# Performance work log

Hardware: AMD Instinct MI355X
Metric: run time of the kernel (lower is better)

The kernel has to match this reference:

```python
import jax, jax.numpy as jnp
import numpy as np

N_NODES = 200000
N_EDGES = 3200000
IN_DIM = 16
EMB_DIM = 8


def setup_inputs() -> dict:
    key = jax.random.key(0)
    ks = jax.random.split(key, 8)
    x = jax.random.normal(ks[0], (N_NODES, IN_DIM), dtype=jnp.float32)
    edge_index = jax.random.randint(ks[1], (2, N_EDGES), 0, N_NODES, dtype=jnp.int32)
    edge_weight = jax.random.uniform(ks[2], (N_EDGES,), dtype=jnp.float32)
    W1_l = jax.random.normal(ks[3], (EMB_DIM, IN_DIM), dtype=jnp.float32) / np.sqrt(IN_DIM)
    W1_r = jax.random.normal(ks[4], (EMB_DIM, IN_DIM), dtype=jnp.float32) / np.sqrt(IN_DIM)
    b1 = jnp.zeros((EMB_DIM,), dtype=jnp.float32)
    W3_l = jax.random.normal(ks[5], (EMB_DIM, EMB_DIM), dtype=jnp.float32) / np.sqrt(EMB_DIM)
    W3_r = jax.random.normal(ks[6], (EMB_DIM, EMB_DIM), dtype=jnp.float32) / np.sqrt(EMB_DIM)
    b3 = jnp.zeros((EMB_DIM,), dtype=jnp.float32)
    return {"x": x, "edge_index": edge_index, "edge_weight": edge_weight,
            "W1_l": W1_l, "W1_r": W1_r, "b1": b1,
            "W3_l": W3_l, "W3_r": W3_r, "b3": b3}


def _sage_conv(x, src, dst, w, W_l, W_r, b):
    # weighted message: x_j * edge_weight, mean-aggregated over in-degree
    n = x.shape[0]
    msg = x[src] * w[:, None]                                  # [E, F]
    agg = jax.ops.segment_sum(msg, dst, num_segments=n)        # [N, F]
    cnt = jax.ops.segment_sum(jnp.ones_like(w), dst, num_segments=n)
    mean = agg / jnp.maximum(cnt, 1.0)[:, None]
    return mean @ W_l.T + x @ W_r.T + b


def reference(x, edge_index, edge_weight, W1_l, W1_r, b1, W3_l, W3_r, b3):
    src, dst = edge_index[0], edge_index[1]
    h = _sage_conv(x, src, dst, edge_weight, W1_l, W1_r, b1)
    h = jax.nn.relu(h)
    # dropout is identity in eval mode
    h = _sage_conv(h, src, dst, edge_weight, W3_l, W3_r, b3)
    return jax.nn.log_softmax(h, axis=1)
```

## Files before the change

kernel.cpp:

```cpp
#include <hip/hip_runtime.h>
#include <hip/hip_fp16.h>
#include <math.h>

#define NN 200000
#define NE 3200000
#define IN_DIM 16
#define EMB 8
#define BK 256
#define NBUK ((NN + BK - 1) / BK)
#define NBLK ((NN + 255) / 256)
#define PLACE_BLOCKS 512
#define PLACE_T 512
#define CHUNK (NE / PLACE_BLOCKS)
#define EPT 13
#define AGG_T 1024
#define CAP 5120
#define RPT 5
#define PRE 4

typedef float vf4 __attribute__((ext_vector_type(4)));
typedef int   vi2 __attribute__((ext_vector_type(2)));

__device__ __forceinline__ void gacc(float* acc, const __half* p, unsigned r)
{
    float w = (float)(r & 63u) * 0.015625f;
    int s = (int)((r >> 6) & 0x3FFFFu);
    vf4 g = *(const vf4*)(p + (size_t)s * EMB);
    union { vf4 f; __half2 h[4]; } u; u.f = g;
    float2 a = __half22float2(u.h[0]);
    float2 c = __half22float2(u.h[1]);
    float2 d = __half22float2(u.h[2]);
    float2 e = __half22float2(u.h[3]);
    acc[0] = fmaf(a.x, w, acc[0]);
    acc[1] = fmaf(a.y, w, acc[1]);
    acc[2] = fmaf(c.x, w, acc[2]);
    acc[3] = fmaf(c.y, w, acc[3]);
    acc[4] = fmaf(d.x, w, acc[4]);
    acc[5] = fmaf(d.y, w, acc[5]);
    acc[6] = fmaf(e.x, w, acc[6]);
    acc[7] = fmaf(e.y, w, acc[7]);
}

__global__ __launch_bounds__(256) void k_init(
    const float* __restrict__ x,
    const float* __restrict__ W1l,
    const float* __restrict__ W1r,
    const float* __restrict__ b1,
    __half* __restrict__ pA, float* __restrict__ t,
    int* __restrict__ bcur)
{
    __shared__ float sWl[EMB * IN_DIM];
    __shared__ float sWr[EMB * IN_DIM];
    __shared__ float sb[EMB];
    int tid = threadIdx.x;
    if (tid < EMB * IN_DIM) { sWl[tid] = W1l[tid]; sWr[tid] = W1r[tid]; }
    if (tid < EMB) sb[tid] = b1[tid];
    __syncthreads();

    int i = blockIdx.x * blockDim.x + tid;
    if (i < NBUK) bcur[i] = i * CAP;
    if (i >= NN) return;

    float xi[IN_DIM];
    const float4* xp = (const float4*)(x + (size_t)i * IN_DIM);
    #pragma unroll
    for (int q = 0; q < 4; ++q) {
        float4 v = xp[q];
        xi[4*q+0] = v.x; xi[4*q+1] = v.y; xi[4*q+2] = v.z; xi[4*q+3] = v.w;
    }

    float pe[EMB], te[EMB];
    #pragma unroll
    for (int e = 0; e < EMB; ++e) {
        float sp = 0.f, st = sb[e];
        #pragma unroll
        for (int k = 0; k < IN_DIM; ++k) {
            sp = fmaf(xi[k], sWl[e * IN_DIM + k], sp);
            st = fmaf(xi[k], sWr[e * IN_DIM + k], st);
        }
        pe[e] = sp; te[e] = st;
    }

    union { vf4 f; __half2 h[4]; } up;
    up.h[0] = __floats2half2_rn(pe[0], pe[1]);
    up.h[1] = __floats2half2_rn(pe[2], pe[3]);
    up.h[2] = __floats2half2_rn(pe[4], pe[5]);
    up.h[3] = __floats2half2_rn(pe[6], pe[7]);
    *(vf4*)(pA + (size_t)i * EMB) = up.f;

    vf4* tp = (vf4*)(t + (size_t)i * EMB);
    vf4 t0 = {te[0], te[1], te[2], te[3]};
    vf4 t1 = {te[4], te[5], te[6], te[7]};
    tp[0] = t0;
    tp[1] = t1;
}

__global__ __launch_bounds__(PLACE_T) void k_bplace(
    const int* __restrict__ src, const int* __restrict__ dst,
    const float* __restrict__ w,
    int* __restrict__ bcur, unsigned* __restrict__ recs)
{
    __shared__ int h[NBUK];
    __shared__ int lb[NBUK];
    __shared__ int gb[NBUK];
    __shared__ int sv[8];
    __shared__ unsigned srec[CHUNK];
    __shared__ unsigned short sbkt[CHUNK];

    int tid = threadIdx.x;
    for (int i = tid; i < NBUK; i += PLACE_T) h[i] = 0;
    __syncthreads();

    int e0 = blockIdx.x * CHUNK;
    int e1 = e0 + CHUNK;

    unsigned rec[EPT];
    int rb[EPT];
    #pragma unroll
    for (int k = 0; k < EPT; ++k) {
        int e = e0 + tid + k * PLACE_T;
        rb[k] = -1;
        if (e < e1) {
            int d = dst[e];
            int b = d >> 8;
            int rank = atomicAdd(&h[b], 1);
            unsigned kq = __float2uint_rn(w[e] * 64.f);
            if (kq > 63u) kq = 63u;
            rec[k] = ((unsigned)(d & (BK - 1)) << 24) | ((unsigned)src[e] << 6) | kq;
            rb[k] = (b << 16) | rank;
        }
    }
    __syncthreads();

    {
        int base2 = tid * 2;
        int s0 = 0, s1 = 0, tot = 0;
        if (base2 + 0 < NBUK) { s0 = tot; tot += h[base2 + 0]; }
        if (base2 + 1 < NBUK) { s1 = tot; tot += h[base2 + 1]; }
        int lane = tid & 63;
        int incl = tot;
        #pragma unroll
        for (int o = 1; o < 64; o <<= 1) {
            int v = __shfl_up(incl, o);
            if (lane >= o) incl += v;
        }
        if (lane == 63) sv[tid >> 6] = incl;
        __syncthreads();
        int wid = tid >> 6;
        int wbase = 0;
        #pragma unroll
        for (int ww = 0; ww < 7; ++ww)
            if (ww < wid) wbase += sv[ww];
        int excl = wbase + incl - tot;
        if (base2 + 0 < NBUK) lb[base2 + 0] = excl + s0;
        if (base2 + 1 < NBUK) lb[base2 + 1] = excl + s1;
    }
    __syncthreads();

    for (int i = tid; i < NBUK; i += PLACE_T) {
        int c = h[i];
        gb[i] = c ? atomicAdd(bcur + i, c) : 0;
    }

    #pragma unroll
    for (int k = 0; k < EPT; ++k) {
        if (rb[k] >= 0) {
            int b = rb[k] >> 16;
            int pos = lb[b] + (rb[k] & 0xFFFF);
            srec[pos] = rec[k];
            sbkt[pos] = (unsigned short)b;
        }
    }
    __syncthreads();

    for (int j = tid; j < CHUNK; j += PLACE_T) {
        int b = sbkt[j];
        recs[gb[b] + (j - lb[b])] = srec[j];
    }
}

__global__ __launch_bounds__(AGG_T) void k_agg1(
    unsigned* __restrict__ recs, const int* __restrict__ bcur,
    const __half* __restrict__ pA, float* __restrict__ t,
    const float* __restrict__ W3l, const float* __restrict__ W3r,
    const float* __restrict__ b3,
    __half* __restrict__ pB, float* __restrict__ invdeg,
    int* __restrict__ soff, int* __restrict__ sdeg)
{
    __shared__ unsigned sbuf[CAP];
    __shared__ int shist[BK];
    __shared__ int sval[4];
    __shared__ int soffl[BK + 1];
    __shared__ float sWl[EMB * EMB];
    __shared__ float sWr[EMB * EMB];
    __shared__ float sb[EMB];

    int tid = threadIdx.x;
    int b = blockIdx.x;
    int bb = b * CAP;
    int cnt = bcur[b] - bb;

    if (tid < EMB * EMB) { sWl[tid] = W3l[tid]; sWr[tid] = W3r[tid]; }
    if (tid < EMB) sb[tid] = b3[tid];
    if (tid < BK) shist[tid] = 0;
    __syncthreads();

    unsigned rec[RPT];
    int rdl[RPT];
    #pragma unroll
    for (int k = 0; k < RPT; ++k) {
        int j = tid + k * AGG_T;
        rdl[k] = -1;
        if (j < cnt) {
            unsigned r = recs[bb + j];
            int dl = (int)(r >> 24);
            int rank = atomicAdd(&shist[dl], 1);
            rec[k] = r;
            rdl[k] = (dl << 16) | rank;
        }
    }
    __syncthreads();

    {
        int v = (tid < BK) ? shist[tid] : 0;
        int lane = tid & 63;
        int incl = v;
        #pragma unroll
        for (int o = 1; o < 64; o <<= 1) {
            int vv = __shfl_up(incl, o);
            if (lane >= o) incl += vv;
        }
        if (tid < BK && lane == 63) sval[tid >> 6] = incl;
        __syncthreads();
        if (tid < BK) {
            int wid = tid >> 6;
            int wbase = 0;
            #pragma unroll
            for (int ww = 0; ww < 3; ++ww)
                if (ww < wid) wbase += sval[ww];
            soffl[tid] = wbase + incl - v;
        }
        if (tid == 0) soffl[BK] = cnt;
    }
    __syncthreads();

    #pragma unroll
    for (int k = 0; k < RPT; ++k) {
        if (rdl[k] >= 0) {
            int dl = rdl[k] >> 16;
            sbuf[soffl[dl] + (rdl[k] & 0xFFFF)] = rec[k];
        }
    }
    __syncthreads();

    for (int p = tid; 2 * p < cnt; p += AGG_T) {
        vi2 q;
        q.x = (int)sbuf[2 * p];
        q.y = (2 * p + 1 < cnt) ? (int)sbuf[2 * p + 1] : 0;
        *(vi2*)(recs + bb + 2 * p) = q;
    }

    int dl = tid >> 2;
    int quarter = tid & 3;
    int i = b * BK + dl;
    bool valid = (i < NN);
    float acc[EMB] = {0.f, 0.f, 0.f, 0.f, 0.f, 0.f, 0.f, 0.f};
    int r0 = 0, r1 = 0;
    if (valid) {
        r0 = soffl[dl];
        r1 = soffl[dl + 1];
        unsigned rr[PRE];
        #pragma unroll
        for (int k = 0; k < PRE; ++k) {
            int j = r0 + quarter + 4 * k;
            rr[k] = (j < r1) ? sbuf[j] : 0u;
        }
        #pragma unroll
        for (int k = 0; k < PRE; ++k) {
            int j = r0 + quarter + 4 * k;
            if (j < r1) gacc(acc, pA, rr[k]);
        }
        for (int j = r0 + quarter + 4 * PRE; j < r1; j += 4) {
            gacc(acc, pA, sbuf[j]);
        }
    }
    #pragma unroll
    for (int e = 0; e < EMB; ++e) {
        acc[e] += __shfl_xor(acc[e], 1);
        acc[e] += __shfl_xor(acc[e], 2);
    }
    if (!valid || quarter) return;

    int deg = r1 - r0;
    soff[i] = bb + r0;
    sdeg[i] = deg;
    float inv = 1.0f / fmaxf((float)deg, 1.0f);
    invdeg[i] = inv;

    vf4* tp = (vf4*)(t + (size_t)i * EMB);
    vf4 t0 = tp[0], t1 = tp[1];

    float h[EMB];
    h[0] = fmaxf(fmaf(acc[0], inv, t0.x), 0.f);
    h[1] = fmaxf(fmaf(acc[1], inv, t0.y), 0.f);
    h[2] = fmaxf(fmaf(acc[2], inv, t0.z), 0.f);
    h[3] = fmaxf(fmaf(acc[3], inv, t0.w), 0.f);
    h[4] = fmaxf(fmaf(acc[4], inv, t1.x), 0.f);
    h[5] = fmaxf(fmaf(acc[5], inv, t1.y), 0.f);
    h[6] = fmaxf(fmaf(acc[6], inv, t1.z), 0.f);
    h[7] = fmaxf(fmaf(acc[7], inv, t1.w), 0.f);

    float pe[EMB], te[EMB];
    #pragma unroll
    for (int o = 0; o < EMB; ++o) {
        float sp = 0.f, st = sb[o];
        #pragma unroll
        for (int k = 0; k < EMB; ++k) {
            sp = fmaf(h[k], sWl[o * EMB + k], sp);
            st = fmaf(h[k], sWr[o * EMB + k], st);
        }
        pe[o] = sp; te[o] = st;
    }

    union { vf4 f; __half2 h2[4]; } up;
    up.h2[0] = __floats2half2_rn(pe[0], pe[1]);
    up.h2[1] = __floats2half2_rn(pe[2], pe[3]);
    up.h2[2] = __floats2half2_rn(pe[4], pe[5]);
    up.h2[3] = __floats2half2_rn(pe[6], pe[7]);
    *(vf4*)(pB + (size_t)i * EMB) = up.f;

    vf4 s0 = {te[0], te[1], te[2], te[3]};
    vf4 s1 = {te[4], te[5], te[6], te[7]};
    tp[0] = s0;
    tp[1] = s1;
}

__global__ __launch_bounds__(256) void k_agg2(
    const unsigned* __restrict__ recs, const int* __restrict__ soff,
    const int* __restrict__ sdeg,
    const __half* __restrict__ pB, const float* __restrict__ t,
    const float* __restrict__ invdeg,
    float* __restrict__ out)
{
    int gid = blockIdx.x * 256 + threadIdx.x;
    int i = gid >> 2;
    int quarter = gid & 3;
    if (i >= NN) return;

    int r0 = soff[i];
    int r1 = r0 + sdeg[i];
    float acc[EMB] = {0.f, 0.f, 0.f, 0.f, 0.f, 0.f, 0.f, 0.f};

    unsigned rr[PRE];
    #pragma unroll
    for (int k = 0; k < PRE; ++k) {
        int j = r0 + quarter + 4 * k;
        rr[k] = (j < r1) ? recs[j] : 0u;
    }
    #pragma unroll
    for (int k = 0; k < PRE; ++k) {
        int j = r0 + quarter + 4 * k;
        if (j < r1) gacc(acc, pB, rr[k]);
    }
    for (int j = r0 + quarter + 4 * PRE; j < r1; j += 4) {
        gacc(acc, pB, recs[j]);
    }

    #pragma unroll
    for (int e = 0; e < EMB; ++e) {
        acc[e] += __shfl_xor(acc[e], 1);
        acc[e] += __shfl_xor(acc[e], 2);
    }
    if (quarter) return;

    float inv = invdeg[i];
    const vf4* tp = (const vf4*)(t + (size_t)i * EMB);
    vf4 t0 = tp[0], t1 = tp[1];

    float z[EMB];
    z[0] = fmaf(acc[0], inv, t0.x);
    z[1] = fmaf(acc[1], inv, t0.y);
    z[2] = fmaf(acc[2], inv, t0.z);
    z[3] = fmaf(acc[3], inv, t0.w);
    z[4] = fmaf(acc[4], inv, t1.x);
    z[5] = fmaf(acc[5], inv, t1.y);
    z[6] = fmaf(acc[6], inv, t1.z);
    z[7] = fmaf(acc[7], inv, t1.w);

    float m = z[0];
    #pragma unroll
    for (int k = 1; k < EMB; ++k) m = fmaxf(m, z[k]);
    float s = 0.f;
    #pragma unroll
    for (int k = 0; k < EMB; ++k) s += expf(z[k] - m);
    float ls = m + logf(s);

    vf4* op = (vf4*)(out + (size_t)i * EMB);
    vf4 o0 = {z[0]-ls, z[1]-ls, z[2]-ls, z[3]-ls};
    vf4 o1 = {z[4]-ls, z[5]-ls, z[6]-ls, z[7]-ls};
    op[0] = o0;
    op[1] = o1;
}

extern "C" void kernel_launch(void* const* d_in, const int* in_sizes, int n_in,
                              void* d_out, int out_size, void* d_ws, size_t ws_size,
                              hipStream_t stream)
{
    const float* x   = (const float*)d_in[0];
    const int*   ei  = (const int*)d_in[1];
    const float* ew  = (const float*)d_in[2];
    const float* W1l = (const float*)d_in[3];
    const float* W1r = (const float*)d_in[4];
    const float* b1  = (const float*)d_in[5];
    const float* W3l = (const float*)d_in[6];
    const float* W3r = (const float*)d_in[7];
    const float* b3  = (const float*)d_in[8];
    float* out = (float*)d_out;

    const int* src = ei;
    const int* dst = ei + NE;

    char* w = (char*)d_ws;
    float*    t     = (float*)w;     w += (size_t)NN * EMB * 4;
    __half*   pA    = (__half*)w;    w += (size_t)NN * EMB * 2;
    __half*   pB    = (__half*)w;    w += (size_t)NN * EMB * 2;
    float*    invd  = (float*)w;     w += (size_t)NN * 4;
    int*      soff  = (int*)w;       w += (size_t)NN * 4;
    int*      sdeg  = (int*)w;       w += (size_t)NN * 4;
    int*      bcur  = (int*)w;       w += (size_t)NBUK * 4;
    w = (char*)(((size_t)w + 15) & ~(size_t)15);
    unsigned* recs  = (unsigned*)w;

    dim3 blk(256);

    k_init<<<dim3(NBLK), blk, 0, stream>>>(x, W1l, W1r, b1, pA, t, bcur);
    k_bplace<<<dim3(PLACE_BLOCKS), dim3(PLACE_T), 0, stream>>>(src, dst, ew, bcur, recs);
    k_agg1<<<dim3(NBUK), dim3(AGG_T), 0, stream>>>(recs, bcur, pA, t, W3l, W3r, b3, pB, invd, soff, sdeg);
    k_agg2<<<dim3((4 * NN + 255) / 256), blk, 0, stream>>>(recs, soff, sdeg, pB, t, invd, out);
}
```

Before: 96.66 us.

## Fuse layer-1 node projection into edge placement and widen agg2 to 8 lanes

The per-node layer-1 projections (pA, t) move out of the separate init kernel and into the bucket-placement kernel, so each placement block also processes its own slice of nodes and only a tiny one-block kernel remains to initialise bucket cursors. This aims to overlap the dense node work with the edge scatter and remove a full-grid launch. Separately, the second aggregation now gives each node 8 lanes instead of 4, with a shallower prefetch and an extra shuffle stage, to raise memory-level parallelism on the gathers. The cost is more threads and more reduction work for low-degree nodes, plus extra registers and shared memory in the placement kernel.

Result: slower. 126.5 us (+30.9%).

```diff
diff --git a/kernel.cpp b/kernel.cpp
--- a/kernel.cpp
+++ b/kernel.cpp
@@ -8,15 +8,16 @@
 #define EMB 8
 #define BK 256
 #define NBUK ((NN + BK - 1) / BK)
-#define NBLK ((NN + 255) / 256)
 #define PLACE_BLOCKS 512
 #define PLACE_T 512
 #define CHUNK (NE / PLACE_BLOCKS)
 #define EPT 13
+#define NPB ((NN + PLACE_BLOCKS - 1) / PLACE_BLOCKS)
 #define AGG_T 1024
 #define CAP 5120
 #define RPT 5
 #define PRE 4
+#define PRE2 2
 
 typedef float vf4 __attribute__((ext_vector_type(4)));
 typedef int   vi2 __attribute__((ext_vector_type(2)));
@@ -41,74 +42,35 @@
     acc[7] = fmaf(e.y, w, acc[7]);
 }
 
-__global__ __launch_bounds__(256) void k_init(
-    const float* __restrict__ x,
-    const float* __restrict__ W1l,
-    const float* __restrict__ W1r,
-    const float* __restrict__ b1,
-    __half* __restrict__ pA, float* __restrict__ t,
-    int* __restrict__ bcur)
-{
-    __shared__ float sWl[EMB * IN_DIM];
-    __shared__ float sWr[EMB * IN_DIM];
-    __shared__ float sb[EMB];
-    int tid = threadIdx.x;
-    if (tid < EMB * IN_DIM) { sWl[tid] = W1l[tid]; sWr[tid] = W1r[tid]; }
-    if (tid < EMB) sb[tid] = b1[tid];
-    __syncthreads();
-
-    int i = blockIdx.x * blockDim.x + tid;
+__global__ __launch_bounds__(1024) void k_zero(int* __restrict__ bcur)
+{
+    int i = threadIdx.x;
     if (i < NBUK) bcur[i] = i * CAP;
-    if (i >= NN) return;
-
-    float xi[IN_DIM];
-    const float4* xp = (const float4*)(x + (size_t)i * IN_DIM);
-    #pragma unroll
-    for (int q = 0; q < 4; ++q) {
-        float4 v = xp[q];
-        xi[4*q+0] = v.x; xi[4*q+1] = v.y; xi[4*q+2] = v.z; xi[4*q+3] = v.w;
-    }
-
-    float pe[EMB], te[EMB];
-    #pragma unroll
-    for (int e = 0; e < EMB; ++e) {
-        float sp = 0.f, st = sb[e];
-        #pragma unroll
-        for (int k = 0; k < IN_DIM; ++k) {
-            sp = fmaf(xi[k], sWl[e * IN_DIM + k], sp);
-            st = fmaf(xi[k], sWr[e * IN_DIM + k], st);
-        }
-        pe[e] = sp; te[e] = st;
-    }
-
-    union { vf4 f; __half2 h[4]; } up;
-    up.h[0] = __floats2half2_rn(pe[0], pe[1]);
-    up.h[1] = __floats2half2_rn(pe[2], pe[3]);
-    up.h[2] = __floats2half2_rn(pe[4], pe[5]);
-    up.h[3] = __floats2half2_rn(pe[6], pe[7]);
-    *(vf4*)(pA + (size_t)i * EMB) = up.f;
-
-    vf4* tp = (vf4*)(t + (size_t)i * EMB);
-    vf4 t0 = {te[0], te[1], te[2], te[3]};
-    vf4 t1 = {te[4], te[5], te[6], te[7]};
-    tp[0] = t0;
-    tp[1] = t1;
 }
 
 __global__ __launch_bounds__(PLACE_T) void k_bplace(
     const int* __restrict__ src, const int* __restrict__ dst,
     const float* __restrict__ w,
+    const float* __restrict__ x,
+    const float* __restrict__ W1l, const float* __restrict__ W1r,
+    const float* __restrict__ b1,
+    __half* __restrict__ pA, float* __restrict__ t,
     int* __restrict__ bcur, unsigned* __restrict__ recs)
 {
     __shared__ int h[NBUK];
     __shared__ int lb[NBUK];
     __shared__ int gb[NBUK];
     __shared__ int sv[8];
+    __shared__ float sWl[EMB * IN_DIM];
+    __shared__ float sWr[EMB * IN_DIM];
+    __shared__ float sb[EMB];
     __shared__ unsigned srec[CHUNK];
     __shared__ unsigned short sbkt[CHUNK];
 
     int tid = threadIdx.x;
     for (int i = tid; i < NBUK; i += PLACE_T) h[i] = 0;
+    if (tid < EMB * IN_DIM) { sWl[tid] = W1l[tid]; sWr[tid] = W1r[tid]; }
+    if (tid < EMB) sb[tid] = b1[tid];
     __syncthreads();
 
     int e0 = blockIdx.x * CHUNK;
@@ -130,6 +92,42 @@
             rb[k] = (b << 16) | rank;
         }
     }
+
+    {
+        int n0 = blockIdx.x * NPB;
+        int nend = n0 + NPB; if (nend > NN) nend = NN;
+        for (int i = n0 + tid; i < nend; i += PLACE_T) {
+            float xi[IN_DIM];
+            const float4* xp = (const float4*)(x + (size_t)i * IN_DIM);
+            #pragma unroll
+            for (int q = 0; q < 4; ++q) {
+                float4 v = xp[q];
+                xi[4*q+0] = v.x; xi[4*q+1] = v.y; xi[4*q+2] = v.z; xi[4*q+3] = v.w;
+            }
+            float pe[EMB], te[EMB];
+            #pragma unroll
+            for (int e = 0; e < EMB; ++e) {
+                float sp = 0.f, st = sb[e];
+                #pragma unroll
+                for (int k = 0; k < IN_DIM; ++k) {
+                    sp = fmaf(xi[k], sWl[e * IN_DIM + k], sp);
+                    st = fmaf(xi[k], sWr[e * IN_DIM + k], st);
+                }
+                pe[e] = sp; te[e] = st;
+            }
+            union { vf4 f; __half2 h2[4]; } up;
+            up.h2[0] = __floats2half2_rn(pe[0], pe[1]);
+            up.h2[1] = __floats2half2_rn(pe[2], pe[3]);
+            up.h2[2] = __floats2half2_rn(pe[4], pe[5]);
+            up.h2[3] = __floats2half2_rn(pe[6], pe[7]);
+            *(vf4*)(pA + (size_t)i * EMB) = up.f;
+            vf4* tp = (vf4*)(t + (size_t)i * EMB);
+            vf4 t0 = {te[0], te[1], te[2], te[3]};
+            vf4 t1 = {te[4], te[5], te[6], te[7]};
+            tp[0] = t0;
+            tp[1] = t1;
+        }
+    }
     __syncthreads();
 
     {
@@ -343,26 +341,26 @@
     float* __restrict__ out)
 {
     int gid = blockIdx.x * 256 + threadIdx.x;
-    int i = gid >> 2;
-    int quarter = gid & 3;
+    int i = gid >> 3;
+    int oct = gid & 7;
     if (i >= NN) return;
 
     int r0 = soff[i];
     int r1 = r0 + sdeg[i];
     float acc[EMB] = {0.f, 0.f, 0.f, 0.f, 0.f, 0.f, 0.f, 0.f};
 
-    unsigned rr[PRE];
-    #pragma unroll
-    for (int k = 0; k < PRE; ++k) {
-        int j = r0 + quarter + 4 * k;
+    unsigned rr[PRE2];
+    #pragma unroll
+    for (int k = 0; k < PRE2; ++k) {
+        int j = r0 + oct + 8 * k;
         rr[k] = (j < r1) ? recs[j] : 0u;
     }
     #pragma unroll
-    for (int k = 0; k < PRE; ++k) {
-        int j = r0 + quarter + 4 * k;
+    for (int k = 0; k < PRE2; ++k) {
+        int j = r0 + oct + 8 * k;
         if (j < r1) gacc(acc, pB, rr[k]);
     }
-    for (int j = r0 + quarter + 4 * PRE; j < r1; j += 4) {
+    for (int j = r0 + oct + 8 * PRE2; j < r1; j += 8) {
         gacc(acc, pB, recs[j]);
     }
 
@@ -370,8 +368,9 @@
     for (int e = 0; e < EMB; ++e) {
         acc[e] += __shfl_xor(acc[e], 1);
         acc[e] += __shfl_xor(acc[e], 2);
-    }
-    if (quarter) return;
+        acc[e] += __shfl_xor(acc[e], 4);
+    }
+    if (oct) return;
 
     float inv = invdeg[i];
     const vf4* tp = (const vf4*)(t + (size_t)i * EMB);
@@ -431,10 +430,9 @@
     w = (char*)(((size_t)w + 15) & ~(size_t)15);
     unsigned* recs  = (unsigned*)w;
 
-    dim3 blk(256);
-
-    k_init<<<dim3(NBLK), blk, 0, stream>>>(x, W1l, W1r, b1, pA, t, bcur);
-    k_bplace<<<dim3(PLACE_BLOCKS), dim3(PLACE_T), 0, stream>>>(src, dst, ew, bcur, recs);
+    k_zero<<<dim3(1), dim3(1024), 0, stream>>>(bcur);
+    k_bplace<<<dim3(PLACE_BLOCKS), dim3(PLACE_T), 0, stream>>>(
+        src, dst, ew, x, W1l, W1r, b1, pA, t, bcur, recs);
     k_agg1<<<dim3(NBUK), dim3(AGG_T), 0, stream>>>(recs, bcur, pA, t, W3l, W3r, b3, pB, invd, soff, sdeg);
-    k_agg2<<<dim3((4 * NN + 255) / 256), blk, 0, stream>>>(recs, soff, sdeg, pB, t, invd, out);
-}
+    k_agg2<<<dim3((8 * NN + 255) / 256), dim3(256), 0, stream>>>(recs, soff, sdeg, pB, t, invd, out);
+}
```
